# Kernel tuning notes

Hardware: AMD Instinct MI355X
Metric: run time of the kernel (lower is better)

Reference implementation:

```python
import jax, jax.numpy as jnp
import numpy as np

N_BUS = 200000; N_GEN = 50000
E_BB = 1600000; E_GB = 400000; E_BG = 400000
D_IN = 64; H = 32
OUT_BUS = 4; OUT_GEN = 2


def setup_inputs() -> dict:
    key = jax.random.key(0)
    it = iter(jax.random.split(key, 48))
    def nrm(shape, s=0.05):
        return jax.random.normal(next(it), shape, jnp.float32) * s
    inp = {}
    inp["x_bus"] = jax.random.normal(next(it), (N_BUS, D_IN), jnp.float32)
    inp["x_gen"] = jax.random.normal(next(it), (N_GEN, D_IN), jnp.float32)
    inp["src_bb"] = jax.random.randint(next(it), (E_BB,), 0, N_BUS)
    inp["dst_bb"] = jax.random.randint(next(it), (E_BB,), 0, N_BUS)
    inp["src_gb"] = jax.random.randint(next(it), (E_GB,), 0, N_GEN)
    inp["dst_gb"] = jax.random.randint(next(it), (E_GB,), 0, N_BUS)
    inp["src_bg"] = jax.random.randint(next(it), (E_BG,), 0, N_BUS)
    inp["dst_bg"] = jax.random.randint(next(it), (E_BG,), 0, N_GEN)
    # SAGEConv params per layer / relation: lin_l (on aggregated neighbors, with bias),
    # lin_r (root weight on x_dst, no bias) -- matches PyG SAGEConv defaults.
    for lname, din in (("l1", D_IN), ("l2", H)):
        for rel in ("bb", "gb", "bg"):
            inp[f"{lname}_{rel}_Wl"] = nrm((din, H))
            inp[f"{lname}_{rel}_bl"] = jnp.zeros((H,), jnp.float32)
            inp[f"{lname}_{rel}_Wr"] = nrm((din, H))
    for nt, dout in (("bus", OUT_BUS), ("gen", OUT_GEN)):
        inp[f"lin0_{nt}_W"] = nrm((H, H))
        inp[f"lin0_{nt}_b"] = jnp.zeros((H,), jnp.float32)
        inp[f"linf_{nt}_W"] = nrm((H, dout))
        inp[f"linf_{nt}_b"] = jnp.zeros((dout,), jnp.float32)
    return inp


def _sage(x_src, x_dst, src, dst, Wl, bl, Wr, n_dst):
    # SAGEConv: mean-aggregate neighbor features, then out = lin_l(mean) + lin_r(x_dst)
    msg = jax.ops.segment_sum(x_src[src], dst, num_segments=n_dst)
    cnt = jax.ops.segment_sum(jnp.ones((src.shape[0],), x_src.dtype), dst, num_segments=n_dst)
    mean = msg / jnp.maximum(cnt, 1.0)[:, None]
    return mean @ Wl + bl + x_dst @ Wr


def reference(x_bus, x_gen, src_bb, dst_bb, src_gb, dst_gb, src_bg, dst_bg,
              l1_bb_Wl, l1_bb_bl, l1_bb_Wr, l1_gb_Wl, l1_gb_bl, l1_gb_Wr,
              l1_bg_Wl, l1_bg_bl, l1_bg_Wr,
              l2_bb_Wl, l2_bb_bl, l2_bb_Wr, l2_gb_Wl, l2_gb_bl, l2_gb_Wr,
              l2_bg_Wl, l2_bg_bl, l2_bg_Wr,
              lin0_bus_W, lin0_bus_b, lin0_gen_W, lin0_gen_b,
              linf_bus_W, linf_bus_b, linf_gen_W, linf_gen_b):
    # HeteroConv layer 1 (aggr='sum' over relations targeting each dst type)
    hb = (_sage(x_bus, x_bus, src_bb, dst_bb, l1_bb_Wl, l1_bb_bl, l1_bb_Wr, N_BUS)
          + _sage(x_gen, x_bus, src_gb, dst_gb, l1_gb_Wl, l1_gb_bl, l1_gb_Wr, N_BUS))
    hg = _sage(x_bus, x_gen, src_bg, dst_bg, l1_bg_Wl, l1_bg_bl, l1_bg_Wr, N_GEN)
    xb, xg = jax.nn.relu(hb), jax.nn.relu(hg)  # dropout is identity in eval mode
    # HeteroConv layer 2
    hb = (_sage(xb, xb, src_bb, dst_bb, l2_bb_Wl, l2_bb_bl, l2_bb_Wr, N_BUS)
          + _sage(xg, xb, src_gb, dst_gb, l2_gb_Wl, l2_gb_bl, l2_gb_Wr, N_BUS))
    hg = _sage(xb, xg, src_bg, dst_bg, l2_bg_Wl, l2_bg_bl, l2_bg_Wr, N_GEN)
    xb, xg = jax.nn.relu(hb), jax.nn.relu(hg)
    # per-node-type hidden Linear (input relu'd again as in the original; relu is idempotent)
    xb = jax.nn.relu(xb) @ lin0_bus_W + lin0_bus_b
    xg = jax.nn.relu(xg) @ lin0_gen_W + lin0_gen_b
    out_bus = xb @ linf_bus_W + linf_bus_b
    out_gen = xg @ linf_gen_W + linf_gen_b
    return out_bus, out_gen
```

## Files before the change

kernel.cpp:

```cpp
#include <hip/hip_runtime.h>
#include <hip/hip_bf16.h>

#define N_BUS 200000
#define N_GEN 50000
#define E_BB 1600000
#define E_GB 400000
#define E_BG 400000
#define H 32
#define NBINS 1024
#define EPT 16

#define NB_CSR_BUS 782
#define NB_CSR_GEN 196
#define NB_PART_BB 391
#define NB_PART_GB 98
#define NB_PART_BG 98
#define NB_TF_BUS 782
#define NB_TF_GEN 196
#define NB_PL_BUS 6250
#define NB_PL_GEN 1563

typedef __attribute__((ext_vector_type(8))) short short8;
typedef __attribute__((ext_vector_type(4))) float floatx4;

__device__ inline unsigned short f2bf(float f) {
    __hip_bfloat16 h = __float2bfloat16(f);
    return *reinterpret_cast<unsigned short*>(&h);
}
__device__ inline float bf2f(unsigned short u) {
    return __uint_as_float(((unsigned)u) << 16);
}


__device__ __forceinline__ void hist_body(int blk, int nb, const int* __restrict__ dst,
                                          int nE, unsigned* __restrict__ bcnt) {
    __shared__ unsigned h[NBINS];
    for (int i = threadIdx.x; i < NBINS; i += 256) h[i] = 0;
    __syncthreads();
    for (int e = blk * 256 + threadIdx.x; e < nE; e += nb * 256)
        atomicAdd(&h[(unsigned)dst[e] >> 8], 1u);
    __syncthreads();
    for (int i = threadIdx.x; i < NBINS; i += 256)
        if (h[i]) atomicAdd(&bcnt[i], h[i]);
}

__global__ __launch_bounds__(256) void hist_all_kernel(
    const int* __restrict__ dbb, const int* __restrict__ dgb, const int* __restrict__ dbg,
    unsigned* __restrict__ cbb, unsigned* __restrict__ cgb, unsigned* __restrict__ cbg)
{
    int b = blockIdx.x;
    if (b < 256) hist_body(b, 256, dbb, E_BB, cbb);
    else if (b < 352) hist_body(b - 256, 96, dgb, E_GB, cgb);
    else hist_body(b - 352, 96, dbg, E_BG, cbg);
}

__global__ __launch_bounds__(256) void scan_all_kernel(unsigned* __restrict__ c0,
                                                       unsigned* __restrict__ c1,
                                                       unsigned* __restrict__ c2) {
    unsigned* a = (blockIdx.x == 0) ? c0 : (blockIdx.x == 1) ? c1 : c2;
    __shared__ unsigned sh[256];
    int tid = threadIdx.x;
    int base = tid * 4;
    unsigned v[4], ts = 0;
#pragma unroll
    for (int q = 0; q < 4; q++) { v[q] = a[base + q]; ts += v[q]; }
    sh[tid] = ts;
    __syncthreads();
#pragma unroll
    for (int d = 1; d < 256; d <<= 1) {
        unsigned t = (tid >= d) ? sh[tid - d] : 0u;
        __syncthreads();
        sh[tid] += t;
        __syncthreads();
    }
    unsigned run = sh[tid] - ts;
#pragma unroll
    for (int q = 0; q < 4; q++) { a[base + q] = run; run += v[q]; }
}

__device__ __forceinline__ void part_body(int blk, const int* __restrict__ src,
                                          const int* __restrict__ dst, int nE,
                                          unsigned* __restrict__ cursor,
                                          unsigned* __restrict__ pairs) {
    __shared__ unsigned hist[NBINS];
    __shared__ unsigned base[NBINS];
    const int tid = threadIdx.x;
    const int cbase = blk * (256 * EPT);

    unsigned es[EPT], ed[EPT];
#pragma unroll
    for (int q = 0; q < EPT; q++) {
        int i = cbase + q * 256 + tid;
        if (i < nE) { es[q] = (unsigned)src[i]; ed[q] = (unsigned)dst[i]; }
        else ed[q] = 0xFFFFFFFFu;
    }
    for (int i = tid; i < NBINS; i += 256) hist[i] = 0;
    __syncthreads();
#pragma unroll
    for (int q = 0; q < EPT; q++)
        if (ed[q] != 0xFFFFFFFFu) atomicAdd(&hist[ed[q] >> 8], 1u);
    __syncthreads();
    for (int i = tid; i < NBINS; i += 256) {
        unsigned c = hist[i];
        base[i] = c ? atomicAdd(&cursor[i], c) : 0u;
        hist[i] = 0;
    }
    __syncthreads();
#pragma unroll
    for (int q = 0; q < EPT; q++) {
        if (ed[q] != 0xFFFFFFFFu) {
            unsigned b = ed[q] >> 8;
            unsigned off = atomicAdd(&hist[b], 1u);
            pairs[base[b] + off] = ((ed[q] & 255u) << 24) | es[q];
        }
    }
}

__global__ __launch_bounds__(256) void part_all_kernel(
    const int* __restrict__ sbb, const int* __restrict__ dbb, unsigned* __restrict__ cbb, unsigned* __restrict__ pbb,
    const int* __restrict__ sgb, const int* __restrict__ dgb, unsigned* __restrict__ cgb, unsigned* __restrict__ pgb,
    const int* __restrict__ sbg, const int* __restrict__ dbg, unsigned* __restrict__ cbg, unsigned* __restrict__ pbg)
{
    int b = blockIdx.x;
    if (b < NB_PART_BB) part_body(b, sbb, dbb, E_BB, cbb, pbb);
    else if (b < NB_PART_BB + NB_PART_GB) part_body(b - NB_PART_BB, sgb, dgb, E_GB, cgb, pgb);
    else part_body(b - NB_PART_BB - NB_PART_GB, sbg, dbg, E_BG, cbg, pbg);
}

__device__ __forceinline__ void fine_body(int b, const unsigned* __restrict__ cursor,
                                          const unsigned* __restrict__ pairs,
                                          unsigned* __restrict__ rs,
                                          unsigned* __restrict__ esrc, int nDst) {
    __shared__ unsigned cnt[256];
    __shared__ unsigned sh[256];
    const int tid = threadIdx.x;
    const unsigned start = b ? cursor[b - 1] : 0u;
    const unsigned end = cursor[b];

    cnt[tid] = 0;
    __syncthreads();
    for (unsigned k = start + tid; k < end; k += 256)
        atomicAdd(&cnt[pairs[k] >> 24], 1u);
    __syncthreads();
    unsigned c = cnt[tid];
    sh[tid] = c;
    __syncthreads();
#pragma unroll
    for (int d = 1; d < 256; d <<= 1) {
        unsigned t = (tid >= d) ? sh[tid - d] : 0u;
        __syncthreads();
        sh[tid] += t;
        __syncthreads();
    }
    int gd = b * 256 + tid;
    if (gd < nDst) rs[gd] = start + sh[tid];
    cnt[tid] = sh[tid] - c;
    __syncthreads();
    for (unsigned k = start + tid; k < end; k += 256) {
        unsigned p = pairs[k];
        unsigned off = atomicAdd(&cnt[p >> 24], 1u);
        esrc[start + off] = p & 0x00FFFFFFu;
    }
}

__global__ __launch_bounds__(256) void fine_all_kernel(
    const unsigned* __restrict__ cbb, const unsigned* __restrict__ pbb, unsigned* __restrict__ rsbb, unsigned* __restrict__ ebb,
    const unsigned* __restrict__ cgb, const unsigned* __restrict__ pgb, unsigned* __restrict__ rsgb, unsigned* __restrict__ egb,
    const unsigned* __restrict__ cbg, const unsigned* __restrict__ pbg, unsigned* __restrict__ rsbg, unsigned* __restrict__ ebg)
{
    int b = blockIdx.x;
    if (b < NB_CSR_BUS) fine_body(b, cbb, pbb, rsbb, ebb, N_BUS);
    else if (b < 2 * NB_CSR_BUS) fine_body(b - NB_CSR_BUS, cgb, pgb, rsgb, egb, N_BUS);
    else fine_body(b - 2 * NB_CSR_BUS, cbg, pbg, rsbg, ebg, N_GEN);
}

__global__ __launch_bounds__(256) void prep_kernel(
    const float* __restrict__ l1_bb_Wl, const float* __restrict__ l1_bb_bl, const float* __restrict__ l1_bb_Wr,
    const float* __restrict__ l1_gb_Wl, const float* __restrict__ l1_gb_bl, const float* __restrict__ l1_gb_Wr,
    const float* __restrict__ l1_bg_Wl, const float* __restrict__ l1_bg_bl, const float* __restrict__ l1_bg_Wr,
    const float* __restrict__ l2_bb_Wl, const float* __restrict__ l2_bb_bl, const float* __restrict__ l2_bb_Wr,
    const float* __restrict__ l2_gb_Wl, const float* __restrict__ l2_gb_bl, const float* __restrict__ l2_gb_Wr,
    const float* __restrict__ l2_bg_Wl, const float* __restrict__ l2_bg_bl, const float* __restrict__ l2_bg_Wr,
    const float* __restrict__ lin0_bus_W, const float* __restrict__ lin0_bus_b,
    const float* __restrict__ linf_bus_W, const float* __restrict__ linf_bus_b,
    const float* __restrict__ lin0_gen_W, const float* __restrict__ lin0_gen_b,
    const float* __restrict__ linf_gen_W, const float* __restrict__ linf_gen_b,
    unsigned short* __restrict__ Wf1b, float* __restrict__ B1b,
    unsigned short* __restrict__ Wf1g, float* __restrict__ B1g,
    unsigned short* __restrict__ Wf2b, float* __restrict__ B2b,
    unsigned short* __restrict__ Wf2g, float* __restrict__ B2g,
    float* __restrict__ WeB, float* __restrict__ beB,
    float* __restrict__ WeG, float* __restrict__ beG)
{
    int t0 = blockIdx.x * 256 + threadIdx.x;
    int NT = gridDim.x * 256;

    for (int f = t0; f < 2 * 6 * 64 * 8; f += NT) {
        int j = f & 7, l = (f >> 3) & 63, tile = f >> 9;
        int nt = tile % 6, kt = tile / 6;
        int k = kt * 32 + (l >> 4) * 8 + j, n = nt * 16 + (l & 15);
        float v;
        if (n < 32) v = l1_bb_Wl[k * 32 + n];
        else if (n < 64) v = l1_bg_Wl[k * 32 + n - 32];
        else v = l1_bb_Wr[k * 32 + n - 64] + l1_gb_Wr[k * 32 + n - 64];
        Wf1b[f] = f2bf(v);
    }
    for (int f = t0; f < 2 * 4 * 64 * 8; f += NT) {
        int j = f & 7, l = (f >> 3) & 63, tile = f >> 9;
        int nt = tile % 4, kt = tile / 4;
        int k = kt * 32 + (l >> 4) * 8 + j, n = nt * 16 + (l & 15);
        float v = (n < 32) ? l1_gb_Wl[k * 32 + n] : l1_bg_Wr[k * 32 + n - 32];
        Wf1g[f] = f2bf(v);
    }
    for (int f = t0; f < 6 * 64 * 8; f += NT) {
        int j = f & 7, l = (f >> 3) & 63, nt = f >> 9;
        int k = (l >> 4) * 8 + j, n = nt * 16 + (l & 15);
        float v;
        if (n < 32) v = l2_bb_Wl[k * 32 + n];
        else if (n < 64) v = l2_bg_Wl[k * 32 + n - 32];
        else v = l2_bb_Wr[k * 32 + n - 64] + l2_gb_Wr[k * 32 + n - 64];
        Wf2b[f] = f2bf(v);
    }
    for (int f = t0; f < 4 * 64 * 8; f += NT) {
        int j = f & 7, l = (f >> 3) & 63, nt = f >> 9;
        int k = (l >> 4) * 8 + j, n = nt * 16 + (l & 15);
        float v = (n < 32) ? l2_gb_Wl[k * 32 + n] : l2_bg_Wr[k * 32 + n - 32];
        Wf2g[f] = f2bf(v);
    }
    if (t0 < 96) {
        B1b[t0] = (t0 < 64) ? 0.0f : l1_bb_bl[t0 - 64] + l1_gb_bl[t0 - 64];
        B2b[t0] = (t0 < 64) ? 0.0f : l2_bb_bl[t0 - 64] + l2_gb_bl[t0 - 64];
    }
    if (t0 < 64) {
        B1g[t0] = (t0 < 32) ? 0.0f : l1_bg_bl[t0 - 32];
        B2g[t0] = (t0 < 32) ? 0.0f : l2_bg_bl[t0 - 32];
    }
    if (t0 < 128) {
        int k = t0 >> 2, c = t0 & 3;
        float s = 0.0f;
        for (int m = 0; m < 32; m++) s += lin0_bus_W[k * 32 + m] * linf_bus_W[m * 4 + c];
        WeB[t0] = s;
    }
    if (t0 >= 128 && t0 < 132) {
        int c = t0 - 128;
        float s = linf_bus_b[c];
        for (int m = 0; m < 32; m++) s += lin0_bus_b[m] * linf_bus_W[m * 4 + c];
        beB[c] = s;
    }
    if (t0 >= 132 && t0 < 196) {
        int i = t0 - 132, k = i >> 1, c = i & 1;
        float s = 0.0f;
        for (int m = 0; m < 32; m++) s += lin0_gen_W[k * 32 + m] * linf_gen_W[m * 2 + c];
        WeG[i] = s;
    }
    if (t0 >= 196 && t0 < 198) {
        int c = t0 - 196;
        float s = linf_gen_b[c];
        for (int m = 0; m < 32; m++) s += lin0_gen_b[m] * linf_gen_W[m * 2 + c];
        beG[c] = s;
    }
}

template <int K, int NOUT, bool RELU_IN>
__device__ __forceinline__ void transform_body(
    int blk, const float* x, int n,
    const unsigned short* __restrict__ Wf, const float* __restrict__ bias,
    unsigned short* __restrict__ y0, unsigned short* __restrict__ y1, float* h,
    char* ldsraw)
{
    constexpr int KT = K / 32, NTN = NOUT / 16, NCH = NOUT / 32;
    constexpr int XS = K + 8;
    constexpr int OS = 34;
    short* lx = (short*)ldsraw;
    float* lo = (float*)ldsraw;

    const int tid = threadIdx.x;
    const int base = blk * 256;
    const int rows = min(256, n - base);
    const int w = tid >> 6, l = tid & 63, quad = l >> 4, ln = l & 15;

    short8 bf[KT][NTN];
    const short8* wf8 = (const short8*)Wf;
#pragma unroll
    for (int kt = 0; kt < KT; kt++)
#pragma unroll
        for (int nt = 0; nt < NTN; nt++)
            bf[kt][nt] = wf8[(kt * NTN + nt) * 64 + l];
    float bv[NTN];
#pragma unroll
    for (int nt = 0; nt < NTN; nt++) bv[nt] = bias[nt * 16 + ln];

    {
        const float4* xg = (const float4*)(x + (size_t)base * K);
        const int T4 = rows * (K / 4);
        for (int q = tid; q < T4; q += 256) {
            float4 v = xg[q];
            if (RELU_IN) {
                v.x = fmaxf(v.x, 0.f); v.y = fmaxf(v.y, 0.f);
                v.z = fmaxf(v.z, 0.f); v.w = fmaxf(v.w, 0.f);
            }
            int r = q / (K / 4), c = (q % (K / 4)) * 4;
            short4 s4;
            s4.x = (short)f2bf(v.x); s4.y = (short)f2bf(v.y);
            s4.z = (short)f2bf(v.z); s4.w = (short)f2bf(v.w);
            *(short4*)&lx[r * XS + c] = s4;
        }
    }
    __syncthreads();

    floatx4 acc[4][NTN];
#pragma unroll
    for (int mt = 0; mt < 4; mt++)
#pragma unroll
        for (int nt = 0; nt < NTN; nt++) {
            floatx4 c0 = {bv[nt], bv[nt], bv[nt], bv[nt]};
            acc[mt][nt] = c0;
        }
#pragma unroll
    for (int mt = 0; mt < 4; mt++) {
        const int row = w * 64 + mt * 16 + ln;
#pragma unroll
        for (int kt = 0; kt < KT; kt++) {
            short8 af = *(const short8*)&lx[row * XS + kt * 32 + quad * 8];
#pragma unroll
            for (int nt = 0; nt < NTN; nt++)
                acc[mt][nt] = __builtin_amdgcn_mfma_f32_16x16x32_bf16(
                    af, bf[kt][nt], acc[mt][nt], 0, 0, 0);
        }
    }

#pragma unroll
    for (int c = 0; c < NCH; c++) {
        __syncthreads();
#pragma unroll
        for (int mt = 0; mt < 4; mt++)
#pragma unroll
            for (int d = 0; d < 2; d++) {
                int nt = 2 * c + d;
#pragma unroll
                for (int r = 0; r < 4; r++)
                    lo[(w * 64 + mt * 16 + quad * 4 + r) * OS + d * 16 + ln] = acc[mt][nt][r];
            }
        __syncthreads();
        const int T4 = rows * 8;
        if (c == NCH - 1) {
            float* og = h + (size_t)base * 32;
            for (int q = tid; q < T4; q += 256) {
                int r = q >> 3, cc = (q & 7) * 4;
                const float* p = &lo[r * OS + cc];
                *(float4*)(og + q * 4) = make_float4(p[0], p[1], p[2], p[3]);
            }
        } else {
            unsigned short* og = ((c == 0) ? y0 : y1) + (size_t)base * 32;
            for (int q = tid; q < T4; q += 256) {
                int r = q >> 3, cc = (q & 7) * 4;
                const float* p = &lo[r * OS + cc];
                short4 s4;
                s4.x = (short)f2bf(p[0]); s4.y = (short)f2bf(p[1]);
                s4.z = (short)f2bf(p[2]); s4.w = (short)f2bf(p[3]);
                *(short4*)(og + q * 4) = s4;
            }
        }
    }
}

template <int K, bool RELU_IN>
__global__ __launch_bounds__(256) void tf_all_kernel(
    const float* xb, const unsigned short* __restrict__ Wfb, const float* __restrict__ Bb,
    unsigned short* __restrict__ yb0, unsigned short* __restrict__ yb1, float* hb,
    const float* xg, const unsigned short* __restrict__ Wfg, const float* __restrict__ Bg,
    unsigned short* __restrict__ yg0, float* hg)
{
    constexpr int XB = 256 * (K + 8) * 2, OB = 256 * 34 * 4;
    __shared__ __align__(16) char ldsraw[(XB > OB) ? XB : OB];
    int b = blockIdx.x;
    if (b < NB_TF_BUS)
        transform_body<K, 96, RELU_IN>(b, xb, N_BUS, Wfb, Bb, yb0, yb1, hb, ldsraw);
    else
        transform_body<K, 64, RELU_IN>(b - NB_TF_BUS, xg, N_GEN, Wfg, Bg, yg0, nullptr, hg, ldsraw);
}

template <bool FUSE>
__device__ __forceinline__ void pull_body(
    int blk, bool hasB, int n,
    const unsigned* __restrict__ rsA, const unsigned* __restrict__ eA, const unsigned short* __restrict__ yA,
    const unsigned* __restrict__ rsB, const unsigned* __restrict__ eB, const unsigned short* __restrict__ yB,
    float* __restrict__ h,
    const float* __restrict__ We, const float* __restrict__ be, int DOUT, float* __restrict__ outp)
{
    const int tid = threadIdx.x;
    unsigned node = blk * 32u + (tid >> 3);
    int j = (tid & 7) * 4;
    if (node >= (unsigned)n) return;

    float4 r = *(const float4*)(h + (size_t)node * H + j);

    auto accum_rel = [&](const unsigned* __restrict__ rs, const unsigned* __restrict__ e,
                         const unsigned short* __restrict__ y) {
        unsigned k0 = node ? rs[node - 1] : 0u;
        unsigned k1 = rs[node];
        float4 a0 = make_float4(0.f, 0.f, 0.f, 0.f);
        float4 a1 = make_float4(0.f, 0.f, 0.f, 0.f);
        float4 a2 = make_float4(0.f, 0.f, 0.f, 0.f);
        float4 a3 = make_float4(0.f, 0.f, 0.f, 0.f);
        unsigned k = k0;
        for (; k + 4 <= k1; k += 4) {
            unsigned s0 = e[k], s1 = e[k + 1], s2 = e[k + 2], s3 = e[k + 3];
            ushort4 v0 = *(const ushort4*)(y + (size_t)s0 * H + j);
            ushort4 v1 = *(const ushort4*)(y + (size_t)s1 * H + j);
            ushort4 v2 = *(const ushort4*)(y + (size_t)s2 * H + j);
            ushort4 v3 = *(const ushort4*)(y + (size_t)s3 * H + j);
            a0.x += bf2f(v0.x); a0.y += bf2f(v0.y); a0.z += bf2f(v0.z); a0.w += bf2f(v0.w);
            a1.x += bf2f(v1.x); a1.y += bf2f(v1.y); a1.z += bf2f(v1.z); a1.w += bf2f(v1.w);
            a2.x += bf2f(v2.x); a2.y += bf2f(v2.y); a2.z += bf2f(v2.z); a2.w += bf2f(v2.w);
            a3.x += bf2f(v3.x); a3.y += bf2f(v3.y); a3.z += bf2f(v3.z); a3.w += bf2f(v3.w);
        }
        for (; k < k1; ++k) {
            unsigned s = e[k];
            const ushort4 v = *(const ushort4*)(y + (size_t)s * H + j);
            a0.x += bf2f(v.x); a0.y += bf2f(v.y); a0.z += bf2f(v.z); a0.w += bf2f(v.w);
        }
        a0.x += a1.x + a2.x + a3.x; a0.y += a1.y + a2.y + a3.y;
        a0.z += a1.z + a2.z + a3.z; a0.w += a1.w + a2.w + a3.w;
        unsigned c = k1 - k0;
        float inv = 1.0f / (float)(c > 1u ? c : 1u);
        r.x += a0.x * inv; r.y += a0.y * inv; r.z += a0.z * inv; r.w += a0.w * inv;
    };

    accum_rel(rsA, eA, yA);
    if (hasB) accum_rel(rsB, eB, yB);

    if (!FUSE) {
        *(float4*)(h + (size_t)node * H + j) = r;
        return;
    }

    float p0 = fmaxf(r.x, 0.f), p1 = fmaxf(r.y, 0.f), p2 = fmaxf(r.z, 0.f), p3 = fmaxf(r.w, 0.f);
    float tot[4];
#pragma unroll
    for (int c = 0; c < 4; c++) {
        if (c < DOUT) {
            tot[c] = p0 * We[(j + 0) * DOUT + c] + p1 * We[(j + 1) * DOUT + c]
                   + p2 * We[(j + 2) * DOUT + c] + p3 * We[(j + 3) * DOUT + c];
        } else tot[c] = 0.f;
    }
#pragma unroll
    for (int mask = 1; mask <= 4; mask <<= 1) {
#pragma unroll
        for (int c = 0; c < 4; c++) tot[c] += __shfl_xor(tot[c], mask);
    }
    if ((tid & 7) == 0) {
        if (DOUT == 4) {
            *(float4*)(outp + (size_t)node * 4) =
                make_float4(tot[0] + be[0], tot[1] + be[1], tot[2] + be[2], tot[3] + be[3]);
        } else {
            *(float2*)(outp + (size_t)node * 2) = make_float2(tot[0] + be[0], tot[1] + be[1]);
        }
    }
}

template <bool FUSE>
__global__ __launch_bounds__(256) void pull_all_kernel(
    const unsigned* __restrict__ rsbb, const unsigned* __restrict__ ebb, const unsigned short* __restrict__ ybb,
    const unsigned* __restrict__ rsgb, const unsigned* __restrict__ egb, const unsigned short* __restrict__ ygb,
    float* __restrict__ hb, const float* __restrict__ WeB, const float* __restrict__ beB,
    const unsigned* __restrict__ rsbg, const unsigned* __restrict__ ebg, const unsigned short* __restrict__ ybg,
    float* __restrict__ hg, const float* __restrict__ WeG, const float* __restrict__ beG,
    float* __restrict__ outp)
{
    int b = blockIdx.x;
    if (b < NB_PL_BUS)
        pull_body<FUSE>(b, true, N_BUS, rsbb, ebb, ybb, rsgb, egb, ygb, hb, WeB, beB, 4, outp);
    else
        pull_body<FUSE>(b - NB_PL_BUS, false, N_GEN, rsbg, ebg, ybg, nullptr, nullptr, nullptr,
                        hg, WeG, beG, 2, outp ? outp + (size_t)N_BUS * 4 : nullptr);
}

extern "C" void kernel_launch(void* const* d_in, const int* in_sizes, int n_in,
                              void* d_out, int out_size, void* d_ws, size_t ws_size,
                              hipStream_t stream) {
    const float* x_bus = (const float*)d_in[0];
    const float* x_gen = (const float*)d_in[1];
    const int* src_bb = (const int*)d_in[2];
    const int* dst_bb = (const int*)d_in[3];
    const int* src_gb = (const int*)d_in[4];
    const int* dst_gb = (const int*)d_in[5];
    const int* src_bg = (const int*)d_in[6];
    const int* dst_bg = (const int*)d_in[7];
    const float* l1_bb_Wl = (const float*)d_in[8];
    const float* l1_bb_bl = (const float*)d_in[9];
    const float* l1_bb_Wr = (const float*)d_in[10];
    const float* l1_gb_Wl = (const float*)d_in[11];
    const float* l1_gb_bl = (const float*)d_in[12];
    const float* l1_gb_Wr = (const float*)d_in[13];
    const float* l1_bg_Wl = (const float*)d_in[14];
    const float* l1_bg_bl = (const float*)d_in[15];
    const float* l1_bg_Wr = (const float*)d_in[16];
    const float* l2_bb_Wl = (const float*)d_in[17];
    const float* l2_bb_bl = (const float*)d_in[18];
    const float* l2_bb_Wr = (const float*)d_in[19];
    const float* l2_gb_Wl = (const float*)d_in[20];
    const float* l2_gb_bl = (const float*)d_in[21];
    const float* l2_gb_Wr = (const float*)d_in[22];
    const float* l2_bg_Wl = (const float*)d_in[23];
    const float* l2_bg_bl = (const float*)d_in[24];
    const float* l2_bg_Wr = (const float*)d_in[25];
    const float* lin0_bus_W = (const float*)d_in[26];
    const float* lin0_bus_b = (const float*)d_in[27];
    const float* linf_bus_W = (const float*)d_in[28];
    const float* linf_bus_b = (const float*)d_in[29];
    const float* lin0_gen_W = (const float*)d_in[30];
    const float* lin0_gen_b = (const float*)d_in[31];
    const float* linf_gen_W = (const float*)d_in[32];
    const float* linf_gen_b = (const float*)d_in[33];

    char* ws = (char*)d_ws;
    size_t off = 0;
    auto alloc = [&](size_t bytes) {
        char* p = ws + off;
        off += (bytes + 255) & ~(size_t)255;
        return p;
    };
    unsigned* rs_bb = (unsigned*)alloc((size_t)N_BUS * 4);
    unsigned* rs_gb = (unsigned*)alloc((size_t)N_BUS * 4);
    unsigned* rs_bg = (unsigned*)alloc((size_t)N_GEN * 4);
    unsigned* cur_bb = (unsigned*)alloc(NBINS * 4);
    unsigned* cur_gb = (unsigned*)alloc(NBINS * 4);
    unsigned* cur_bg = (unsigned*)alloc(NBINS * 4);
    unsigned* e_bb = (unsigned*)alloc((size_t)E_BB * 4);
    unsigned* e_gb = (unsigned*)alloc((size_t)E_GB * 4);
    unsigned* e_bg = (unsigned*)alloc((size_t)E_BG * 4);
    unsigned short* y_bb = (unsigned short*)alloc((size_t)N_BUS * H * 2);
    unsigned short* y_bg = (unsigned short*)alloc((size_t)N_BUS * H * 2);
    unsigned short* y_gb = (unsigned short*)alloc((size_t)N_GEN * H * 2);
    float* h_bus = (float*)alloc((size_t)N_BUS * H * 4);
    float* h_gen = (float*)alloc((size_t)N_GEN * H * 4);
    unsigned short* Wf1b = (unsigned short*)alloc(2 * 6 * 64 * 8 * 2);
    float* B1b = (float*)alloc(96 * 4);
    unsigned short* Wf1g = (unsigned short*)alloc(2 * 4 * 64 * 8 * 2);
    float* B1g = (float*)alloc(64 * 4);
    unsigned short* Wf2b = (unsigned short*)alloc(6 * 64 * 8 * 2);
    float* B2b = (float*)alloc(96 * 4);
    unsigned short* Wf2g = (unsigned short*)alloc(4 * 64 * 8 * 2);
    float* B2g = (float*)alloc(64 * 4);
    float* WeB = (float*)alloc(128 * 4);
    float* beB = (float*)alloc(4 * 4);
    float* WeG = (float*)alloc(64 * 4);
    float* beG = (float*)alloc(2 * 4);

    unsigned* p_bb = (unsigned*)y_bb;
    unsigned* p_gb = (unsigned*)y_bg;
    unsigned* p_bg = (unsigned*)y_gb;

    prep_kernel<<<32, 256, 0, stream>>>(
        l1_bb_Wl, l1_bb_bl, l1_bb_Wr, l1_gb_Wl, l1_gb_bl, l1_gb_Wr,
        l1_bg_Wl, l1_bg_bl, l1_bg_Wr, l2_bb_Wl, l2_bb_bl, l2_bb_Wr,
        l2_gb_Wl, l2_gb_bl, l2_gb_Wr, l2_bg_Wl, l2_bg_bl, l2_bg_Wr,
        lin0_bus_W, lin0_bus_b, linf_bus_W, linf_bus_b,
        lin0_gen_W, lin0_gen_b, linf_gen_W, linf_gen_b,
        Wf1b, B1b, Wf1g, B1g, Wf2b, B2b, Wf2g, B2g, WeB, beB, WeG, beG);

    hipMemsetAsync(cur_bb, 0, 3 * NBINS * 4, stream);

    hist_all_kernel<<<448, 256, 0, stream>>>(dst_bb, dst_gb, dst_bg, cur_bb, cur_gb, cur_bg);
    scan_all_kernel<<<3, 256, 0, stream>>>(cur_bb, cur_gb, cur_bg);
    part_all_kernel<<<NB_PART_BB + NB_PART_GB + NB_PART_BG, 256, 0, stream>>>(
        src_bb, dst_bb, cur_bb, p_bb, src_gb, dst_gb, cur_gb, p_gb, src_bg, dst_bg, cur_bg, p_bg);
    fine_all_kernel<<<2 * NB_CSR_BUS + NB_CSR_GEN, 256, 0, stream>>>(
        cur_bb, p_bb, rs_bb, e_bb, cur_gb, p_gb, rs_gb, e_gb, cur_bg, p_bg, rs_bg, e_bg);

    tf_all_kernel<64, false><<<NB_TF_BUS + NB_TF_GEN, 256, 0, stream>>>(
        x_bus, Wf1b, B1b, y_bb, y_bg, h_bus, x_gen, Wf1g, B1g, y_gb, h_gen);
    pull_all_kernel<false><<<NB_PL_BUS + NB_PL_GEN, 256, 0, stream>>>(
        rs_bb, e_bb, y_bb, rs_gb, e_gb, y_gb, h_bus, WeB, beB,
        rs_bg, e_bg, y_bg, h_gen, WeG, beG, nullptr);

    tf_all_kernel<32, true><<<NB_TF_BUS + NB_TF_GEN, 256, 0, stream>>>(
        h_bus, Wf2b, B2b, y_bb, y_bg, h_bus, h_gen, Wf2g, B2g, y_gb, h_gen);
    pull_all_kernel<true><<<NB_PL_BUS + NB_PL_GEN, 256, 0, stream>>>(
        rs_bb, e_bb, y_bb, rs_gb, e_gb, y_gb, h_bus, WeB, beB,
        rs_bg, e_bg, y_bg, h_gen, WeG, beG, (float*)d_out);
}
```

Baseline: 365.8 us.

## Fuse edge partitioning with layer-1 transform and zero cursors in prep kernel

The edge partition step and the layer-1 node transform, which are independent, now run as block ranges of one kernel so they execute concurrently. The partition output buffers were aliased onto the y buffers, so they are moved to separate allocations to remove that conflict. The memset of the bin cursors is folded into the prep kernel, removing a launch. The fused kernel uses the larger LDS footprint for every block, which may lower occupancy for the partition blocks, and it needs extra memory for the pair buffers.

```diff
diff --git a/kernel.cpp b/kernel.cpp
--- a/kernel.cpp
+++ b/kernel.cpp
@@ -15,8 +15,10 @@
 #define NB_PART_BB 391
 #define NB_PART_GB 98
 #define NB_PART_BG 98
+#define NB_PART_ALL 587
 #define NB_TF_BUS 782
 #define NB_TF_GEN 196
+#define NB_TF_ALL 978
 #define NB_PL_BUS 6250
 #define NB_PL_GEN 1563
 
@@ -81,9 +83,8 @@
 __device__ __forceinline__ void part_body(int blk, const int* __restrict__ src,
                                           const int* __restrict__ dst, int nE,
                                           unsigned* __restrict__ cursor,
-                                          unsigned* __restrict__ pairs) {
-    __shared__ unsigned hist[NBINS];
-    __shared__ unsigned base[NBINS];
+                                          unsigned* __restrict__ pairs,
+                                          unsigned* hist, unsigned* base) {
     const int tid = threadIdx.x;
     const int cbase = blk * (256 * EPT);
 
@@ -114,17 +115,6 @@
             pairs[base[b] + off] = ((ed[q] & 255u) << 24) | es[q];
         }
     }
-}
-
-__global__ __launch_bounds__(256) void part_all_kernel(
-    const int* __restrict__ sbb, const int* __restrict__ dbb, unsigned* __restrict__ cbb, unsigned* __restrict__ pbb,
-    const int* __restrict__ sgb, const int* __restrict__ dgb, unsigned* __restrict__ cgb, unsigned* __restrict__ pgb,
-    const int* __restrict__ sbg, const int* __restrict__ dbg, unsigned* __restrict__ cbg, unsigned* __restrict__ pbg)
-{
-    int b = blockIdx.x;
-    if (b < NB_PART_BB) part_body(b, sbb, dbb, E_BB, cbb, pbb);
-    else if (b < NB_PART_BB + NB_PART_GB) part_body(b - NB_PART_BB, sgb, dgb, E_GB, cgb, pgb);
-    else part_body(b - NB_PART_BB - NB_PART_GB, sbg, dbg, E_BG, cbg, pbg);
 }
 
 __device__ __forceinline__ void fine_body(int b, const unsigned* __restrict__ cursor,
@@ -190,10 +180,13 @@
     unsigned short* __restrict__ Wf2b, float* __restrict__ B2b,
     unsigned short* __restrict__ Wf2g, float* __restrict__ B2g,
     float* __restrict__ WeB, float* __restrict__ beB,
-    float* __restrict__ WeG, float* __restrict__ beG)
+    float* __restrict__ WeG, float* __restrict__ beG,
+    unsigned* __restrict__ cursors)
 {
     int t0 = blockIdx.x * 256 + threadIdx.x;
     int NT = gridDim.x * 256;
+
+    if (t0 < 3 * NBINS) cursors[t0] = 0u;
 
     for (int f = t0; f < 2 * 6 * 64 * 8; f += NT) {
         int j = f & 7, l = (f >> 3) & 63, tile = f >> 9;
@@ -364,20 +357,46 @@
     }
 }
 
-template <int K, bool RELU_IN>
-__global__ __launch_bounds__(256) void tf_all_kernel(
+__global__ __launch_bounds__(256) void part_tf1_kernel(
+    const int* __restrict__ sbb, const int* __restrict__ dbb, unsigned* __restrict__ cbb, unsigned* __restrict__ pbb,
+    const int* __restrict__ sgb, const int* __restrict__ dgb, unsigned* __restrict__ cgb, unsigned* __restrict__ pgb,
+    const int* __restrict__ sbg, const int* __restrict__ dbg, unsigned* __restrict__ cbg, unsigned* __restrict__ pbg,
     const float* xb, const unsigned short* __restrict__ Wfb, const float* __restrict__ Bb,
     unsigned short* __restrict__ yb0, unsigned short* __restrict__ yb1, float* hb,
     const float* xg, const unsigned short* __restrict__ Wfg, const float* __restrict__ Bg,
     unsigned short* __restrict__ yg0, float* hg)
 {
-    constexpr int XB = 256 * (K + 8) * 2, OB = 256 * 34 * 4;
+    constexpr int XB = 256 * (64 + 8) * 2, OB = 256 * 34 * 4;
+    __shared__ __align__(16) char ldsraw[(XB > OB) ? XB : OB];
+    int b = blockIdx.x;
+    if (b < NB_PART_ALL) {
+        unsigned* hist = (unsigned*)ldsraw;
+        unsigned* base = hist + NBINS;
+        if (b < NB_PART_BB) part_body(b, sbb, dbb, E_BB, cbb, pbb, hist, base);
+        else if (b < NB_PART_BB + NB_PART_GB) part_body(b - NB_PART_BB, sgb, dgb, E_GB, cgb, pgb, hist, base);
+        else part_body(b - NB_PART_BB - NB_PART_GB, sbg, dbg, E_BG, cbg, pbg, hist, base);
+    } else {
+        int tb = b - NB_PART_ALL;
+        if (tb < NB_TF_BUS)
+            transform_body<64, 96, false>(tb, xb, N_BUS, Wfb, Bb, yb0, yb1, hb, ldsraw);
+        else
+            transform_body<64, 64, false>(tb - NB_TF_BUS, xg, N_GEN, Wfg, Bg, yg0, nullptr, hg, ldsraw);
+    }
+}
+
+__global__ __launch_bounds__(256) void tf2_all_kernel(
+    const float* xb, const unsigned short* __restrict__ Wfb, const float* __restrict__ Bb,
+    unsigned short* __restrict__ yb0, unsigned short* __restrict__ yb1, float* hb,
+    const float* xg, const unsigned short* __restrict__ Wfg, const float* __restrict__ Bg,
+    unsigned short* __restrict__ yg0, float* hg)
+{
+    constexpr int XB = 256 * (32 + 8) * 2, OB = 256 * 34 * 4;
     __shared__ __align__(16) char ldsraw[(XB > OB) ? XB : OB];
     int b = blockIdx.x;
     if (b < NB_TF_BUS)
-        transform_body<K, 96, RELU_IN>(b, xb, N_BUS, Wfb, Bb, yb0, yb1, hb, ldsraw);
+        transform_body<32, 96, true>(b, xb, N_BUS, Wfb, Bb, yb0, yb1, hb, ldsraw);
     else
-        transform_body<K, 64, RELU_IN>(b - NB_TF_BUS, xg, N_GEN, Wfg, Bg, yg0, nullptr, hg, ldsraw);
+        transform_body<32, 64, true>(b - NB_TF_BUS, xg, N_GEN, Wfg, Bg, yg0, nullptr, hg, ldsraw);
 }
 
 template <bool FUSE>
@@ -548,9 +567,9 @@
     float* WeG = (float*)alloc(64 * 4);
     float* beG = (float*)alloc(2 * 4);
 
-    unsigned* p_bb = (unsigned*)y_bb;
-    unsigned* p_gb = (unsigned*)y_bg;
-    unsigned* p_bg = (unsigned*)y_gb;
+    unsigned* p_bb = (unsigned*)alloc((size_t)E_BB * 4);
+    unsigned* p_gb = (unsigned*)alloc((size_t)E_GB * 4);
+    unsigned* p_bg = (unsigned*)alloc((size_t)E_BG * 4);
 
     prep_kernel<<<32, 256, 0, stream>>>(
         l1_bb_Wl, l1_bb_bl, l1_bb_Wr, l1_gb_Wl, l1_gb_bl, l1_gb_Wr,
@@ -558,24 +577,22 @@
         l2_gb_Wl, l2_gb_bl, l2_gb_Wr, l2_bg_Wl, l2_bg_bl, l2_bg_Wr,
         lin0_bus_W, lin0_bus_b, linf_bus_W, linf_bus_b,
         lin0_gen_W, lin0_gen_b, linf_gen_W, linf_gen_b,
-        Wf1b, B1b, Wf1g, B1g, Wf2b, B2b, Wf2g, B2g, WeB, beB, WeG, beG);
-
-    hipMemsetAsync(cur_bb, 0, 3 * NBINS * 4, stream);
+        Wf1b, B1b, Wf1g, B1g, Wf2b, B2b, Wf2g, B2g, WeB, beB, WeG, beG,
+        cur_bb);
 
     hist_all_kernel<<<448, 256, 0, stream>>>(dst_bb, dst_gb, dst_bg, cur_bb, cur_gb, cur_bg);
     scan_all_kernel<<<3, 256, 0, stream>>>(cur_bb, cur_gb, cur_bg);
-    part_all_kernel<<<NB_PART_BB + NB_PART_GB + NB_PART_BG, 256, 0, stream>>>(
-        src_bb, dst_bb, cur_bb, p_bb, src_gb, dst_gb, cur_gb, p_gb, src_bg, dst_bg, cur_bg, p_bg);
+    part_tf1_kernel<<<NB_PART_ALL + NB_TF_ALL, 256, 0, stream>>>(
+        src_bb, dst_bb, cur_bb, p_bb, src_gb, dst_gb, cur_gb, p_gb, src_bg, dst_bg, cur_bg, p_bg,
+        x_bus, Wf1b, B1b, y_bb, y_bg, h_bus, x_gen, Wf1g, B1g, y_gb, h_gen);
     fine_all_kernel<<<2 * NB_CSR_BUS + NB_CSR_GEN, 256, 0, stream>>>(
         cur_bb, p_bb, rs_bb, e_bb, cur_gb, p_gb, rs_gb, e_gb, cur_bg, p_bg, rs_bg, e_bg);
 
-    tf_all_kernel<64, false><<<NB_TF_BUS + NB_TF_GEN, 256, 0, stream>>>(
-        x_bus, Wf1b, B1b, y_bb, y_bg, h_bus, x_gen, Wf1g, B1g, y_gb, h_gen);
     pull_all_kernel<false><<<NB_PL_BUS + NB_PL_GEN, 256, 0, stream>>>(
         rs_bb, e_bb, y_bb, rs_gb, e_gb, y_gb, h_bus, WeB, beB,
         rs_bg, e_bg, y_bg, h_gen, WeG, beG, nullptr);
 
-    tf_all_kernel<32, true><<<NB_TF_BUS + NB_TF_GEN, 256, 0, stream>>>(
+    tf2_all_kernel<<<NB_TF_BUS + NB_TF_GEN, 256, 0, stream>>>(
         h_bus, Wf2b, B2b, y_bb, y_bg, h_bus, h_gen, Wf2g, B2g, y_gb, h_gen);
     pull_all_kernel<true><<<NB_PL_BUS + NB_PL_GEN, 256, 0, stream>>>(
         rs_bb, e_bb, y_bb, rs_gb, e_gb, y_gb, h_bus, WeB, beB,
```

New measurement: 365.9 us. No clear change (+0.0%).
